# Kernel optimization log

Hardware: AMD Instinct MI355X
Metric: run time of the kernel (lower is better)

The kernel has to match this reference:

```python
import jax, jax.numpy as jnp
import numpy as np

N_ATOMS = 200000
N_EDGES = 800000
ATOM_FDIM = 133
HIDDEN = 256
NUM_MOLS = 8000
ALPHA = 0.2  # LeakyReLU slope


def setup_inputs() -> dict:
    key = jax.random.key(0)
    ks = jax.random.split(key, 10)
    f_atoms = jax.random.normal(ks[0], (N_ATOMS, ATOM_FDIM), dtype=jnp.float32)
    edge_index = jax.random.randint(ks[1], (2, N_EDGES), 0, N_ATOMS, dtype=jnp.int64)
    mol_ids = jnp.sort(jax.random.randint(ks[2], (N_ATOMS,), 0, NUM_MOLS, dtype=jnp.int64))
    s0 = 1.0 / np.sqrt(ATOM_FDIM)
    sh = 1.0 / np.sqrt(HIDDEN)
    sa = 1.0 / np.sqrt(2 * HIDDEN)
    W0 = jax.random.normal(ks[3], (ATOM_FDIM, HIDDEN), dtype=jnp.float32) * s0
    a0 = jax.random.normal(ks[4], (2 * HIDDEN,), dtype=jnp.float32) * sa
    W1 = jax.random.normal(ks[5], (HIDDEN, HIDDEN), dtype=jnp.float32) * sh
    a1 = jax.random.normal(ks[6], (2 * HIDDEN,), dtype=jnp.float32) * sa
    W2 = jax.random.normal(ks[7], (HIDDEN, HIDDEN), dtype=jnp.float32) * sh
    a2 = jax.random.normal(ks[8], (2 * HIDDEN,), dtype=jnp.float32) * sa
    return {"f_atoms": f_atoms, "edge_index": edge_index, "mol_ids": mol_ids,
            "W0": W0, "a0": a0, "W1": W1, "a1": a1, "W2": W2, "a2": a2}


def _gat_layer(x, W, a, src, tgt, residual):
    # x: [N, Fin], W: [Fin, H], a: [2H]
    h = x @ W                              # [N, H]
    H = h.shape[1]
    a_s, a_t = a[:H], a[H:]
    # e = leakyrelu([h_src || h_tgt] @ a), computed without materializing the concat
    e = jax.nn.leaky_relu(h[src] @ a_s + h[tgt] @ a_t, negative_slope=ALPHA)  # [E]
    att = jnp.exp(e)
    denom = jax.ops.segment_sum(att, tgt, num_segments=x.shape[0])            # [N]
    att_n = att / (denom[tgt] + 1e-8)
    # weighted scatter-aggregate (dropout is a no-op in eval mode)
    h_prime = jax.ops.segment_sum(h[src] * att_n[:, None], tgt, num_segments=x.shape[0])
    if residual:
        h_prime = h_prime + x
    return jax.nn.elu(h_prime)


def reference(f_atoms, edge_index, mol_ids, W0, a0, W1, a1, W2, a2):
    src, tgt = edge_index[0], edge_index[1]
    x = _gat_layer(f_atoms, W0, a0, src, tgt, residual=False)
    x = _gat_layer(x, W1, a1, src, tgt, residual=True)
    x = _gat_layer(x, W2, a2, src, tgt, residual=True)
    # per-molecule mean pooling (a_scope loop -> segment mean)
    sums = jax.ops.segment_sum(x, mol_ids, num_segments=NUM_MOLS)            # [M, H]
    counts = jax.ops.segment_sum(jnp.ones((x.shape[0],), x.dtype), mol_ids, num_segments=NUM_MOLS)
    return jnp.where(counts[:, None] > 0, sums / jnp.maximum(counts[:, None], 1.0), 0.0)
```

## Files before the change

### kernel.cpp

```cpp
#include <hip/hip_runtime.h>

#define N_ATOMS 200000
#define N_EDGES 800000
#define FDIM    133
#define HID     256
#define NMOLS   8000
#define CAP     32

typedef unsigned short bf16_t;
typedef __attribute__((ext_vector_type(4))) float f32x4;
typedef __attribute__((ext_vector_type(8))) short bf16x8;

__device__ inline float bf2f(bf16_t u) {
    union { unsigned int i; float f; } v; v.i = ((unsigned int)u) << 16; return v.f;
}
__device__ inline bf16_t f2bf(float f) {
    union { float f; unsigned int i; } v; v.f = f;
    return (bf16_t)((v.i + 0x7fffu + ((v.i >> 16) & 1u)) >> 16);
}
__device__ inline float4 ld4(const bf16_t* p) {
    ushort4 u = *(const ushort4*)p;
    return make_float4(bf2f(u.x), bf2f(u.y), bf2f(u.z), bf2f(u.w));
}

__device__ inline void gload_lds16(const void* g, void* l) {
    __builtin_amdgcn_global_load_lds((const __attribute__((address_space(1))) unsigned int*)g,
                                     (__attribute__((address_space(3))) unsigned int*)l,
                                     16, 0, 0);
}

__global__ __launch_bounds__(256) void build_adj(const int* __restrict__ ei,
                                                 int* __restrict__ cnt,
                                                 int* __restrict__ lst) {
    int e = blockIdx.x * 256 + threadIdx.x;
    if (e >= N_EDGES) return;
    int s = ei[e];
    int t = ei[N_EDGES + e];
    int p = atomicAdd(&cnt[t], 1);
    if (p < CAP) lst[t * CAP + p] = s;
}

__global__ __launch_bounds__(256) void transpose_w(const float* __restrict__ W,
                                                   bf16_t* __restrict__ Wt,
                                                   int K, int Kpad) {
    int idx = blockIdx.x * 256 + threadIdx.x;
    if (idx >= HID * Kpad) return;
    int n = idx / Kpad, k = idx - n * Kpad;
    Wt[idx] = (k < K) ? f2bf(W[k * HID + n]) : (bf16_t)0;
}

template <bool A_FP32, int KSTEPS, int LDA, int KP>
__global__ __launch_bounds__(256, 5) void gemm_mfma(const void* __restrict__ Av,
                                                    const bf16_t* __restrict__ Wt,
                                                    bf16_t* __restrict__ H,
                                                    const float* __restrict__ avec,
                                                    float* __restrict__ ssp,
                                                    float* __restrict__ stp) {
    __shared__ bf16_t As[2][64][32];
    __shared__ bf16_t Bs[2][128][32];
    __shared__ float  red[2][64][2];
    const int tid  = threadIdx.x;
    const int lane = tid & 63;
    const int w    = tid >> 6;
    const int wr   = w >> 1;
    const int wc   = w & 1;
    const int fr   = lane & 15;
    const int kg   = lane >> 4;
    const int row0 = blockIdx.x * 64;
    const int n0   = blockIdx.y * 128;

    const int sra  = tid >> 2;
    const int ska  = (tid & 3) * 8;
    const int sgrow = row0 + sra;

    float sreg[8];

#define ISSUE(ks_, buf_) do {                                                          \
    const int k0_ = (ks_) * 32;                                                        \
    if constexpr (A_FP32) {                                                            \
        _Pragma("unroll")                                                              \
        for (int j = 0; j < 8; ++j) {                                                  \
            int gk = k0_ + ska + j;                                                    \
            sreg[j] = (gk < LDA) ? ((const float*)Av)[(long long)sgrow * LDA + gk] : 0.f; \
        }                                                                              \
    } else {                                                                           \
        gload_lds16((const bf16_t*)Av + (long long)sgrow * LDA + k0_ + ska,            \
                    (char*)&As[buf_][0][0] + w * 1024);                                \
    }                                                                                  \
    gload_lds16(Wt + (long long)(n0 + (tid >> 2)) * KP + k0_ + ska,                    \
                (char*)&Bs[buf_][0][0] + w * 1024);                                    \
    gload_lds16(Wt + (long long)(n0 + 64 + (tid >> 2)) * KP + k0_ + ska,               \
                (char*)&Bs[buf_][0][0] + 4096 + w * 1024);                             \
} while (0)

#define COMMIT(buf_) do {                                                              \
    if constexpr (A_FP32) {                                                            \
        short v_[8];                                                                   \
        _Pragma("unroll")                                                              \
        for (int j = 0; j < 8; ++j) v_[j] = (short)f2bf(sreg[j]);                      \
        *(bf16x8*)&As[buf_][sra][ska] = *(bf16x8*)&v_[0];                              \
    }                                                                                  \
} while (0)

#define READ_FRAGS(buf_, af_, bf_) do {                                                \
    const int koff_ = kg * 8;                                                          \
    _Pragma("unroll")                                                                  \
    for (int i = 0; i < 2; ++i)                                                        \
        af_[i] = *(const bf16x8*)&As[buf_][wr * 32 + i * 16 + fr][koff_];              \
    _Pragma("unroll")                                                                  \
    for (int jn = 0; jn < 4; ++jn)                                                     \
        bf_[jn] = *(const bf16x8*)&Bs[buf_][wc * 64 + jn * 16 + fr][koff_];            \
} while (0)

#define DO_MFMA(af_, bf_) do {                                                         \
    _Pragma("unroll")                                                                  \
    for (int i = 0; i < 2; ++i)                                                        \
        _Pragma("unroll")                                                              \
        for (int jn = 0; jn < 4; ++jn)                                                 \
            acc[i][jn] = __builtin_amdgcn_mfma_f32_16x16x32_bf16(af_[i], bf_[jn], acc[i][jn], 0, 0, 0); \
} while (0)

    f32x4 acc[2][4] = {};

    if constexpr (A_FP32) {
        ISSUE(0, 0);
        COMMIT(0);
        __syncthreads();
        int buf = 0;
        for (int ks = 0; ks < KSTEPS; ++ks) {
            if (ks + 1 < KSTEPS) ISSUE(ks + 1, buf ^ 1);
            bf16x8 af[2], bfr[4];
            READ_FRAGS(buf, af, bfr);
            DO_MFMA(af, bfr);
            if (ks + 1 < KSTEPS) COMMIT(buf ^ 1);
            __syncthreads();
            buf ^= 1;
        }
    } else {
        ISSUE(0, 0);
        int buf = 0;
        for (int ks = 0; ks < KSTEPS; ++ks) {
            if (ks + 1 < KSTEPS) {
                ISSUE(ks + 1, buf ^ 1);
                asm volatile("s_waitcnt vmcnt(3)" ::: "memory");
            } else {
                asm volatile("s_waitcnt vmcnt(0)" ::: "memory");
            }
            __builtin_amdgcn_s_barrier();

            bf16x8 af[2], bfr[4];
            READ_FRAGS(buf, af, bfr);
            asm volatile("s_waitcnt lgkmcnt(0)" ::: "memory");
            __builtin_amdgcn_sched_barrier(0);
            __builtin_amdgcn_s_barrier();

            DO_MFMA(af, bfr);
            buf ^= 1;
        }
    }
#undef ISSUE
#undef COMMIT
#undef READ_FRAGS
#undef DO_MFMA

    float as_v[4], at_v[4];
    #pragma unroll
    for (int jn = 0; jn < 4; ++jn) {
        int c = n0 + wc * 64 + jn * 16 + fr;
        as_v[jn] = avec[c];
        at_v[jn] = avec[HID + c];
    }
    #pragma unroll
    for (int i = 0; i < 2; ++i) {
        #pragma unroll
        for (int rr = 0; rr < 4; ++rr) {
            int row_l = wr * 32 + i * 16 + kg * 4 + rr;
            int r = row0 + row_l;
            float ps = 0.f, pt = 0.f;
            #pragma unroll
            for (int jn = 0; jn < 4; ++jn) {
                float h = acc[i][jn][rr];
                ps += h * as_v[jn];
                pt += h * at_v[jn];
                H[(long long)r * HID + (n0 + wc * 64 + jn * 16 + fr)] = f2bf(h);
            }
            #pragma unroll
            for (int o = 1; o < 16; o <<= 1) {
                ps += __shfl_xor(ps, o);
                pt += __shfl_xor(pt, o);
            }
            if (fr == 0) {
                red[0][row_l][wc] = ps;
                red[1][row_l][wc] = pt;
            }
        }
    }
    __syncthreads();
    if (tid < 64) {
        int r = row0 + tid;
        long long slot = (long long)blockIdx.y * N_ATOMS + r;
        ssp[slot] = red[0][tid][0] + red[0][tid][1];
        stp[slot] = red[1][tid][0] + red[1][tid][1];
    }
}

__global__ __launch_bounds__(256) void combine_dots(const float* __restrict__ ssp,
                                                    const float* __restrict__ stp,
                                                    float* __restrict__ ss,
                                                    float* __restrict__ st) {
    int i = blockIdx.x * 256 + threadIdx.x;
    if (i >= N_ATOMS) return;
    ss[i] = ssp[i] + ssp[N_ATOMS + i];
    st[i] = stp[i] + stp[N_ATOMS + i];
}

__global__ __launch_bounds__(256) void aggregate(const bf16_t* __restrict__ H,
                                                 const float* __restrict__ ss,
                                                 const float* __restrict__ st,
                                                 const int* __restrict__ cnt,
                                                 const int* __restrict__ lst,
                                                 bf16_t* __restrict__ X,
                                                 int residual) {
    const int tid  = threadIdx.x;
    const int lane = tid & 63;
    const int wv   = (blockIdx.x * 256 + tid) >> 6;
    const int half = lane >> 5;
    const int sub  = lane & 31;
    const int t    = 2 * wv + half;

    int n = cnt[t]; if (n > CAP) n = CAP;

    const float stt = st[t];
    const unsigned rowoff = (unsigned)t * (HID * 2);
    const unsigned loff   = (unsigned)sub * 16;
    const unsigned lbase  = (unsigned)t * (CAP * 4);

    float acc[8] = {0.f, 0.f, 0.f, 0.f, 0.f, 0.f, 0.f, 0.f};
    float denom = 0.f;

    for (int i0 = 0; i0 < n; i0 += 4) {
        int4 s4 = *(const int4*)((const char*)lst + (lbase + (unsigned)i0 * 4));
        int s0 = s4.x;
        int s1 = (i0 + 1 < n) ? s4.y : s4.x;
        int s2 = (i0 + 2 < n) ? s4.z : s4.x;
        int s3 = (i0 + 3 < n) ? s4.w : s4.x;

        float v0 = ss[s0], v1 = ss[s1], v2 = ss[s2], v3 = ss[s3];

        bf16x8 r0 = *(const bf16x8*)((const char*)H + ((unsigned)s0 * 512u + loff));
        bf16x8 r1 = *(const bf16x8*)((const char*)H + ((unsigned)s1 * 512u + loff));
        bf16x8 r2 = *(const bf16x8*)((const char*)H + ((unsigned)s2 * 512u + loff));
        bf16x8 r3 = *(const bf16x8*)((const char*)H + ((unsigned)s3 * 512u + loff));

        float e0 = v0 + stt; e0 = e0 > 0.f ? e0 : 0.2f * e0;
        float e1 = v1 + stt; e1 = e1 > 0.f ? e1 : 0.2f * e1;
        float e2 = v2 + stt; e2 = e2 > 0.f ? e2 : 0.2f * e2;
        float e3 = v3 + stt; e3 = e3 > 0.f ? e3 : 0.2f * e3;

        float w0 = __expf(e0);
        float w1 = (i0 + 1 < n) ? __expf(e1) : 0.f;
        float w2 = (i0 + 2 < n) ? __expf(e2) : 0.f;
        float w3 = (i0 + 3 < n) ? __expf(e3) : 0.f;

        denom += (w0 + w1) + (w2 + w3);
        #pragma unroll
        for (int e = 0; e < 8; ++e) {
            acc[e] += w0 * bf2f((bf16_t)r0[e]) + w1 * bf2f((bf16_t)r1[e])
                    + w2 * bf2f((bf16_t)r2[e]) + w3 * bf2f((bf16_t)r3[e]);
        }
    }

    const float inv = 1.f / (denom + 1e-8f);
    float r[8];
    #pragma unroll
    for (int e = 0; e < 8; ++e) r[e] = acc[e] * inv;

    if (residual) {
        bf16x8 xv = *(const bf16x8*)((const char*)X + (rowoff + loff));
        #pragma unroll
        for (int e = 0; e < 8; ++e) r[e] += bf2f((bf16_t)xv[e]);
    }

    bf16x8 o;
    #pragma unroll
    for (int e = 0; e < 8; ++e) {
        float x = r[e];
        x = x > 0.f ? x : (__expf(x) - 1.f);
        o[e] = (short)f2bf(x);
    }
    *(bf16x8*)((char*)X + (rowoff + loff)) = o;
}

__device__ inline int lower_bound_i(const int* a, int n, int v) {
    int lo = 0, hi = n;
    while (lo < hi) { int mid = (lo + hi) >> 1; if (a[mid] < v) lo = mid + 1; else hi = mid; }
    return lo;
}

__global__ __launch_bounds__(64) void pool_kernel(const bf16_t* __restrict__ X,
                                                  const int* __restrict__ mol,
                                                  float* __restrict__ out) {
    int m = blockIdx.x;
    int lane = threadIdx.x;
    int lo = lower_bound_i(mol, N_ATOMS, m);
    int hi = lower_bound_i(mol, N_ATOMS, m + 1);
    float ax = 0.f, ay = 0.f, az = 0.f, aw = 0.f;
    for (int i = lo; i < hi; ++i) {
        float4 v = ld4(&X[(long long)i * HID + lane * 4]);
        ax += v.x; ay += v.y; az += v.z; aw += v.w;
    }
    float c = (float)(hi - lo);
    float4 r = make_float4(0.f, 0.f, 0.f, 0.f);
    if (c > 0.f) {
        float inv = 1.f / c;
        r = make_float4(ax * inv, ay * inv, az * inv, aw * inv);
    }
    *(float4*)&out[(long long)m * HID + lane * 4] = r;
}

extern "C" void kernel_launch(void* const* d_in, const int* in_sizes, int n_in,
                              void* d_out, int out_size, void* d_ws, size_t ws_size,
                              hipStream_t stream) {
    const float* f_atoms = (const float*)d_in[0];
    const int*   ei      = (const int*)d_in[1];
    const int*   mol     = (const int*)d_in[2];
    const float* W0      = (const float*)d_in[3];
    const float* a0      = (const float*)d_in[4];
    const float* W1      = (const float*)d_in[5];
    const float* a1      = (const float*)d_in[6];
    const float* W2      = (const float*)d_in[7];
    const float* a2      = (const float*)d_in[8];
    float* out = (float*)d_out;

    char* ws = (char*)d_ws;
    size_t off = 0;
    bf16_t* X  = (bf16_t*)(ws + off); off += (size_t)N_ATOMS * HID * 2;
    bf16_t* Hb = (bf16_t*)(ws + off); off += (size_t)N_ATOMS * HID * 2;
    float* ss  = (float*)(ws + off);  off += (size_t)N_ATOMS * 4;
    float* st  = (float*)(ws + off);  off += (size_t)N_ATOMS * 4;
    int* cnt   = (int*)(ws + off);    off += (size_t)N_ATOMS * 4;
    int* lst   = (int*)(ws + off);    off += (size_t)N_ATOMS * CAP * 4;
    if (ws_size < off) return;

    char* ob = (char*)d_out;
    bf16_t* Wt  = (bf16_t*)ob;
    float*  ssp = (float*)(ob + 131072);
    float*  stp = (float*)(ob + 131072 + 1600000);

    hipMemsetAsync(cnt, 0, (size_t)N_ATOMS * 4, stream);
    build_adj<<<(N_EDGES + 255) / 256, 256, 0, stream>>>(ei, cnt, lst);

    const dim3 gemm_grid(N_ATOMS / 64, 2);
    const int  agg_blocks = N_ATOMS / 8;
    const int  cmb_blocks = (N_ATOMS + 255) / 256;

    transpose_w<<<(HID * 160 + 255) / 256, 256, 0, stream>>>(W0, Wt, FDIM, 160);
    gemm_mfma<true, 5, FDIM, 160><<<gemm_grid, 256, 0, stream>>>(f_atoms, Wt, Hb, a0, ssp, stp);
    combine_dots<<<cmb_blocks, 256, 0, stream>>>(ssp, stp, ss, st);
    aggregate<<<agg_blocks, 256, 0, stream>>>(Hb, ss, st, cnt, lst, X, 0);

    transpose_w<<<(HID * HID + 255) / 256, 256, 0, stream>>>(W1, Wt, HID, HID);
    gemm_mfma<false, 8, HID, HID><<<gemm_grid, 256, 0, stream>>>(X, Wt, Hb, a1, ssp, stp);
    combine_dots<<<cmb_blocks, 256, 0, stream>>>(ssp, stp, ss, st);
    aggregate<<<agg_blocks, 256, 0, stream>>>(Hb, ss, st, cnt, lst, X, 1);

    transpose_w<<<(HID * HID + 255) / 256, 256, 0, stream>>>(W2, Wt, HID, HID);
    gemm_mfma<false, 8, HID, HID><<<gemm_grid, 256, 0, stream>>>(X, Wt, Hb, a2, ssp, stp);
    combine_dots<<<cmb_blocks, 256, 0, stream>>>(ssp, stp, ss, st);
    aggregate<<<agg_blocks, 256, 0, stream>>>(Hb, ss, st, cnt, lst, X, 1);

    pool_kernel<<<NMOLS, 64, 0, stream>>>(X, mol, out);
}
```

Measured before the change: 570.9 us.

## Preload whole weight panel into LDS and stream A fragments directly from global

The GEMM now loads the full 128-column weight panel (all K) into LDS once per block with an XOR swizzle for K=256, then reads A fragments straight from global memory into registers with no LDS staging and no per-K-step barriers. Blocks grow to 512 threads covering 128 rows, with bounds guards for the ragged last tile. This removes the double-buffered pipeline and its synchronisation overhead, but gives up coalesced A loads and raises LDS use per block (64KB for K=256), which may limit occupancy.

```diff
diff --git a/kernel.cpp b/kernel.cpp
--- a/kernel.cpp
+++ b/kernel.cpp
@@ -50,15 +50,15 @@
 }
 
 template <bool A_FP32, int KSTEPS, int LDA, int KP>
-__global__ __launch_bounds__(256, 5) void gemm_mfma(const void* __restrict__ Av,
+__global__ __launch_bounds__(512, 4) void gemm_mfma(const void* __restrict__ Av,
                                                     const bf16_t* __restrict__ Wt,
                                                     bf16_t* __restrict__ H,
                                                     const float* __restrict__ avec,
                                                     float* __restrict__ ssp,
                                                     float* __restrict__ stp) {
-    __shared__ bf16_t As[2][64][32];
-    __shared__ bf16_t Bs[2][128][32];
-    __shared__ float  red[2][64][2];
+    constexpr bool SWZ = (KP == 256);
+    __shared__ bf16_t Bs[128 * KP];
+    __shared__ float  red[2][128][2];
     const int tid  = threadIdx.x;
     const int lane = tid & 63;
     const int w    = tid >> 6;
@@ -66,102 +66,74 @@
     const int wc   = w & 1;
     const int fr   = lane & 15;
     const int kg   = lane >> 4;
-    const int row0 = blockIdx.x * 64;
+    const int row0 = blockIdx.x * 128;
     const int n0   = blockIdx.y * 128;
 
-    const int sra  = tid >> 2;
-    const int ska  = (tid & 3) * 8;
-    const int sgrow = row0 + sra;
-
-    float sreg[8];
-
-#define ISSUE(ks_, buf_) do {                                                          \
-    const int k0_ = (ks_) * 32;                                                        \
-    if constexpr (A_FP32) {                                                            \
-        _Pragma("unroll")                                                              \
-        for (int j = 0; j < 8; ++j) {                                                  \
-            int gk = k0_ + ska + j;                                                    \
-            sreg[j] = (gk < LDA) ? ((const float*)Av)[(long long)sgrow * LDA + gk] : 0.f; \
-        }                                                                              \
-    } else {                                                                           \
-        gload_lds16((const bf16_t*)Av + (long long)sgrow * LDA + k0_ + ska,            \
-                    (char*)&As[buf_][0][0] + w * 1024);                                \
-    }                                                                                  \
-    gload_lds16(Wt + (long long)(n0 + (tid >> 2)) * KP + k0_ + ska,                    \
-                (char*)&Bs[buf_][0][0] + w * 1024);                                    \
-    gload_lds16(Wt + (long long)(n0 + 64 + (tid >> 2)) * KP + k0_ + ska,               \
-                (char*)&Bs[buf_][0][0] + 4096 + w * 1024);                             \
-} while (0)
-
-#define COMMIT(buf_) do {                                                              \
-    if constexpr (A_FP32) {                                                            \
-        short v_[8];                                                                   \
-        _Pragma("unroll")                                                              \
-        for (int j = 0; j < 8; ++j) v_[j] = (short)f2bf(sreg[j]);                      \
-        *(bf16x8*)&As[buf_][sra][ska] = *(bf16x8*)&v_[0];                              \
-    }                                                                                  \
-} while (0)
-
-#define READ_FRAGS(buf_, af_, bf_) do {                                                \
-    const int koff_ = kg * 8;                                                          \
-    _Pragma("unroll")                                                                  \
-    for (int i = 0; i < 2; ++i)                                                        \
-        af_[i] = *(const bf16x8*)&As[buf_][wr * 32 + i * 16 + fr][koff_];              \
-    _Pragma("unroll")                                                                  \
-    for (int jn = 0; jn < 4; ++jn)                                                     \
-        bf_[jn] = *(const bf16x8*)&Bs[buf_][wc * 64 + jn * 16 + fr][koff_];            \
-} while (0)
-
-#define DO_MFMA(af_, bf_) do {                                                         \
-    _Pragma("unroll")                                                                  \
-    for (int i = 0; i < 2; ++i)                                                        \
-        _Pragma("unroll")                                                              \
-        for (int jn = 0; jn < 4; ++jn)                                                 \
-            acc[i][jn] = __builtin_amdgcn_mfma_f32_16x16x32_bf16(af_[i], bf_[jn], acc[i][jn], 0, 0, 0); \
-} while (0)
+    {
+        const char* panel = (const char*)Wt + (long long)n0 * (KP * 2);
+        #pragma unroll
+        for (int it = 0; it < KSTEPS; ++it) {
+            int u = it * 8192 + tid * 16;
+            int src;
+            if constexpr (SWZ) {
+                int col = u >> 9;
+                int kb  = u & 511;
+                src = (col << 9) + (kb ^ ((col & 7) << 4));
+            } else {
+                src = u;
+            }
+            gload_lds16(panel + src, (char*)Bs + it * 8192 + w * 1024);
+        }
+    }
+    __syncthreads();
 
     f32x4 acc[2][4] = {};
-
-    if constexpr (A_FP32) {
-        ISSUE(0, 0);
-        COMMIT(0);
-        __syncthreads();
-        int buf = 0;
-        for (int ks = 0; ks < KSTEPS; ++ks) {
-            if (ks + 1 < KSTEPS) ISSUE(ks + 1, buf ^ 1);
-            bf16x8 af[2], bfr[4];
-            READ_FRAGS(buf, af, bfr);
-            DO_MFMA(af, bfr);
-            if (ks + 1 < KSTEPS) COMMIT(buf ^ 1);
-            __syncthreads();
-            buf ^= 1;
-        }
-    } else {
-        ISSUE(0, 0);
-        int buf = 0;
-        for (int ks = 0; ks < KSTEPS; ++ks) {
-            if (ks + 1 < KSTEPS) {
-                ISSUE(ks + 1, buf ^ 1);
-                asm volatile("s_waitcnt vmcnt(3)" ::: "memory");
-            } else {
-                asm volatile("s_waitcnt vmcnt(0)" ::: "memory");
-            }
-            __builtin_amdgcn_s_barrier();
-
-            bf16x8 af[2], bfr[4];
-            READ_FRAGS(buf, af, bfr);
-            asm volatile("s_waitcnt lgkmcnt(0)" ::: "memory");
-            __builtin_amdgcn_sched_barrier(0);
-            __builtin_amdgcn_s_barrier();
-
-            DO_MFMA(af, bfr);
-            buf ^= 1;
-        }
-    }
-#undef ISSUE
-#undef COMMIT
-#undef READ_FRAGS
-#undef DO_MFMA
+    int ar[2];
+    #pragma unroll
+    for (int i = 0; i < 2; ++i) {
+        int r = row0 + wr * 32 + i * 16 + fr;
+        ar[i] = (r < N_ATOMS) ? r : (N_ATOMS - 1);
+    }
+
+    #pragma unroll
+    for (int ks = 0; ks < KSTEPS; ++ks) {
+        const int kbase = ks * 32 + kg * 8;
+        bf16x8 af[2], bf[4];
+
+        if constexpr (A_FP32) {
+            const float* A = (const float*)Av;
+            #pragma unroll
+            for (int i = 0; i < 2; ++i) {
+                const float* src = A + (long long)ar[i] * LDA + kbase;
+                short v[8];
+                #pragma unroll
+                for (int j = 0; j < 8; ++j)
+                    v[j] = (kbase + j < LDA) ? (short)f2bf(src[j]) : (short)0;
+                af[i] = *(bf16x8*)v;
+            }
+        } else {
+            const bf16_t* A = (const bf16_t*)Av;
+            #pragma unroll
+            for (int i = 0; i < 2; ++i)
+                af[i] = *(const bf16x8*)(A + (long long)ar[i] * LDA + kbase);
+        }
+
+        #pragma unroll
+        for (int jn = 0; jn < 4; ++jn) {
+            int col = wc * 64 + jn * 16 + fr;
+            int kb  = kbase * 2;
+            int off;
+            if constexpr (SWZ) off = (col << 9) + (kb ^ ((col & 7) << 4));
+            else               off = col * (KP * 2) + kb;
+            bf[jn] = *(const bf16x8*)((const char*)Bs + off);
+        }
+
+        #pragma unroll
+        for (int i = 0; i < 2; ++i)
+            #pragma unroll
+            for (int jn = 0; jn < 4; ++jn)
+                acc[i][jn] = __builtin_amdgcn_mfma_f32_16x16x32_bf16(af[i], bf[jn], acc[i][jn], 0, 0, 0);
+    }
 
     float as_v[4], at_v[4];
     #pragma unroll
@@ -182,7 +154,8 @@
                 float h = acc[i][jn][rr];
                 ps += h * as_v[jn];
                 pt += h * at_v[jn];
-                H[(long long)r * HID + (n0 + wc * 64 + jn * 16 + fr)] = f2bf(h);
+                if (r < N_ATOMS)
+                    H[(long long)r * HID + (n0 + wc * 64 + jn * 16 + fr)] = f2bf(h);
             }
             #pragma unroll
             for (int o = 1; o < 16; o <<= 1) {
@@ -196,11 +169,13 @@
         }
     }
     __syncthreads();
-    if (tid < 64) {
+    if (tid < 128) {
         int r = row0 + tid;
-        long long slot = (long long)blockIdx.y * N_ATOMS + r;
-        ssp[slot] = red[0][tid][0] + red[0][tid][1];
-        stp[slot] = red[1][tid][0] + red[1][tid][1];
+        if (r < N_ATOMS) {
+            long long slot = (long long)blockIdx.y * N_ATOMS + r;
+            ssp[slot] = red[0][tid][0] + red[0][tid][1];
+            stp[slot] = red[1][tid][0] + red[1][tid][1];
+        }
     }
 }
 
@@ -350,22 +325,22 @@
     hipMemsetAsync(cnt, 0, (size_t)N_ATOMS * 4, stream);
     build_adj<<<(N_EDGES + 255) / 256, 256, 0, stream>>>(ei, cnt, lst);
 
-    const dim3 gemm_grid(N_ATOMS / 64, 2);
+    const dim3 gemm_grid((N_ATOMS + 127) / 128, 2);
     const int  agg_blocks = N_ATOMS / 8;
     const int  cmb_blocks = (N_ATOMS + 255) / 256;
 
     transpose_w<<<(HID * 160 + 255) / 256, 256, 0, stream>>>(W0, Wt, FDIM, 160);
-    gemm_mfma<true, 5, FDIM, 160><<<gemm_grid, 256, 0, stream>>>(f_atoms, Wt, Hb, a0, ssp, stp);
+    gemm_mfma<true, 5, FDIM, 160><<<gemm_grid, 512, 0, stream>>>(f_atoms, Wt, Hb, a0, ssp, stp);
     combine_dots<<<cmb_blocks, 256, 0, stream>>>(ssp, stp, ss, st);
     aggregate<<<agg_blocks, 256, 0, stream>>>(Hb, ss, st, cnt, lst, X, 0);
 
     transpose_w<<<(HID * HID + 255) / 256, 256, 0, stream>>>(W1, Wt, HID, HID);
-    gemm_mfma<false, 8, HID, HID><<<gemm_grid, 256, 0, stream>>>(X, Wt, Hb, a1, ssp, stp);
+    gemm_mfma<false, 8, HID, HID><<<gemm_grid, 512, 0, stream>>>(X, Wt, Hb, a1, ssp, stp);
     combine_dots<<<cmb_blocks, 256, 0, stream>>>(ssp, stp, ss, st);
     aggregate<<<agg_blocks, 256, 0, stream>>>(Hb, ss, st, cnt, lst, X, 1);
 
     transpose_w<<<(HID * HID + 255) / 256, 256, 0, stream>>>(W2, Wt, HID, HID);
-    gemm_mfma<false, 8, HID, HID><<<gemm_grid, 256, 0, stream>>>(X, Wt, Hb, a2, ssp, stp);
+    gemm_mfma<false, 8, HID, HID><<<gemm_grid, 512, 0, stream>>>(X, Wt, Hb, a2, ssp, stp);
     combine_dots<<<cmb_blocks, 256, 0, stream>>>(ssp, stp, ss, st);
     aggregate<<<agg_blocks, 256, 0, stream>>>(Hb, ss, st, cnt, lst, X, 1);
 
```

New measurement: 616.4 us. +8.0%, slower.
